# Kernel tuning notes

Hardware: AMD Instinct MI355X
Metric: run time of the kernel (lower is better)

Reference implementation:

```python
import jax, jax.numpy as jnp
import numpy as np

B, I, N = 1024, 128, 256
UNFOLDS = 6  # ode_solver_unfolds


def _sig(v, mu, sigma):
    # v: [B, D] -> [B, D, 1]; mu/sigma: [D, N] -> broadcast [B, D, N]
    return jax.nn.sigmoid(sigma * (v[..., None] - mu))


def setup_inputs() -> dict:
    key = jax.random.key(0)
    ks = jax.random.split(key, 12)
    u = lambda k, shape, lo, hi: jax.random.uniform(k, shape, jnp.float32, lo, hi)
    pm1 = lambda k, shape: (2.0 * jax.random.randint(k, shape, 0, 2) - 1.0).astype(jnp.float32)
    return {
        "inputs": jax.random.normal(ks[0], (B, I), jnp.float32),
        "state": jax.random.normal(ks[1], (B, N), jnp.float32) * 0.1,
        "input_w": jnp.ones((I,), jnp.float32),
        "input_b": jnp.zeros((I,), jnp.float32),
        "sensory_mu": u(ks[2], (I, N), 0.3, 0.8),
        "sensory_sigma": u(ks[3], (I, N), 3.0, 8.0),
        "sensory_W": u(ks[4], (I, N), 0.01, 1.0),
        "sensory_erev": pm1(ks[5], (I, N)),
        "mu": u(ks[6], (N, N), 0.3, 0.8),
        "sigma": u(ks[7], (N, N), 3.0, 8.0),
        "W": u(ks[8], (N, N), 0.01, 1.0),
        "erev": pm1(ks[9], (N, N)),
        "vleak": u(ks[10], (N,), -0.2, 0.2),
        "gleak": jnp.ones((N,), jnp.float32),   # gleak_init_min == gleak_init_max == 1.0
        "cm_t": jnp.full((N,), 0.5, jnp.float32),  # cm_init_min == cm_init_max == 0.5
    }


def reference(inputs, state, input_w, input_b, sensory_mu, sensory_sigma,
              sensory_W, sensory_erev, mu, sigma, W, erev, vleak, gleak, cm_t):
    # Affine input mapping
    x = inputs * input_w + input_b  # [B, I]
    # Sensory synapse activations (constant across unfolds)
    s_act = sensory_W * _sig(x, sensory_mu, sensory_sigma)  # [B, I, N]
    w_num_sensory = jnp.sum(s_act * sensory_erev, axis=1)   # [B, N]
    w_den_sensory = jnp.sum(s_act, axis=1)                  # [B, N]

    def step(v_pre, _):
        w_act = W * _sig(v_pre, mu, sigma)                  # [B, N, N]
        w_num = jnp.sum(w_act * erev, axis=1) + w_num_sensory
        w_den = jnp.sum(w_act, axis=1) + w_den_sensory
        numerator = cm_t * v_pre + gleak * vleak + w_num
        denominator = cm_t + gleak + w_den
        return numerator / denominator, None

    v_pre, _ = jax.lax.scan(step, state, None, length=UNFOLDS)
    # module returns (outputs, next_state) with outputs == next_state
    return v_pre
```

## Files before the change

### kernel.cpp

```cpp
#include <hip/hip_runtime.h>


#define LOG2E 1.44269504088896340f

constexpr int Bn = 1024;
constexpr int In = 128;
constexpr int Nn = 256;
constexpr int UNFOLDS = 6;

#if __has_builtin(__builtin_amdgcn_exp2f)
#define EXP2F(x) __builtin_amdgcn_exp2f(x)
#else
#define EXP2F(x) __exp2f(x)
#endif
#if __has_builtin(__builtin_amdgcn_rcpf)
#define RCPF(x) __builtin_amdgcn_rcpf(x)
#else
#define RCPF(x) (1.0f / (x))
#endif

__global__ __launch_bounds__(256) void pack_kernel(
    const float* __restrict__ mu, const float* __restrict__ sigma,
    const float* __restrict__ W, const float* __restrict__ erev,
    const float* __restrict__ smu, const float* __restrict__ ssigma,
    const float* __restrict__ sW, const float* __restrict__ serev,
    float4* __restrict__ Prec, float4* __restrict__ Psen) {
    int idx = blockIdx.x * 256 + threadIdx.x;
    if (idx < Nn * Nn) {
        float s = sigma[idx], m = mu[idx], w = W[idx], e = erev[idx];
        Prec[idx] = make_float4(s * LOG2E, s * m * LOG2E, w, w * e);
        return;
    }
    int j = idx - Nn * Nn;
    if (j < In * Nn) {
        float s = ssigma[j], m = smu[j], w = sW[j], e = serev[j];
        Psen[j] = make_float4(s * LOG2E, s * m * LOG2E, w, w * e);
    }
}

__global__ __launch_bounds__(256) void sensory_kernel(
    const float* __restrict__ inputs, const float* __restrict__ input_w,
    const float* __restrict__ input_b, const float4* __restrict__ Psen,
    float2* __restrict__ sens) {
    __shared__ float4 xs[In];
    __shared__ float2 part[4][4][64];

    const int tid = threadIdx.x;
    const int b0 = (blockIdx.x >> 2) * 4;
    const int n0 = (blockIdx.x & 3) * 64;

    for (int k = tid; k < 4 * In; k += 256) {
        int i = k >> 2, bb = k & 3;
        ((float*)xs)[i * 4 + bb] =
            inputs[(b0 + bb) * In + i] * input_w[i] + input_b[i];
    }
    __syncthreads();

    const int n_l = tid & 63;
    const int sl = tid >> 6;
    const float4* __restrict__ pp = Psen + n0 + n_l;

    float num[4] = {0.f, 0.f, 0.f, 0.f};
    float den[4] = {0.f, 0.f, 0.f, 0.f};
#pragma unroll 4
    for (int i = sl * 32; i < sl * 32 + 32; ++i) {
        float4 p = pp[i * Nn];
        float4 v = xs[i];
#pragma unroll
        for (int bb = 0; bb < 4; ++bb) {
            float vb = (bb == 0) ? v.x : (bb == 1) ? v.y : (bb == 2) ? v.z : v.w;
            float r = RCPF(1.0f + EXP2F(fmaf(-p.x, vb, p.y)));
            den[bb] += p.z * r;
            num[bb] += p.w * r;
        }
    }
#pragma unroll
    for (int bb = 0; bb < 4; ++bb)
        part[sl][bb][n_l] = make_float2(num[bb], den[bb]);
    __syncthreads();

    const int bb = tid >> 6, nl2 = tid & 63;
    float wn = 0.f, wd = 0.f;
#pragma unroll
    for (int s = 0; s < 4; ++s) {
        float2 v = part[s][bb][nl2];
        wn += v.x;
        wd += v.y;
    }
    sens[(b0 + bb) * Nn + n0 + nl2] = make_float2(wn, wd);
}

__global__ __launch_bounds__(256) void step_kernel(
    const float* __restrict__ vcur, const float4* __restrict__ Prec,
    const float2* __restrict__ sens, const float* __restrict__ vleak,
    const float* __restrict__ gleak, const float* __restrict__ cmt,
    float* __restrict__ vnext) {
    __shared__ float4 vt[Nn];
    __shared__ float2 part[4][4][64];

    const int tid = threadIdx.x;
    const int b0 = (blockIdx.x >> 2) * 4;
    const int n0 = (blockIdx.x & 3) * 64;

    for (int k = tid; k < 4 * Nn; k += 256) {
        int i = k >> 2, bb = k & 3;
        ((float*)vt)[i * 4 + bb] = vcur[(b0 + bb) * Nn + i];
    }
    __syncthreads();

    const int n_l = tid & 63;
    const int sl = tid >> 6;
    const float4* __restrict__ pp = Prec + n0 + n_l;

    float num[4] = {0.f, 0.f, 0.f, 0.f};
    float den[4] = {0.f, 0.f, 0.f, 0.f};
#pragma unroll 4
    for (int i = sl * 64; i < sl * 64 + 64; ++i) {
        float4 p = pp[i * Nn];
        float4 v = vt[i];
#pragma unroll
        for (int bb = 0; bb < 4; ++bb) {
            float vb = (bb == 0) ? v.x : (bb == 1) ? v.y : (bb == 2) ? v.z : v.w;
            float r = RCPF(1.0f + EXP2F(fmaf(-p.x, vb, p.y)));
            den[bb] += p.z * r;
            num[bb] += p.w * r;
        }
    }
#pragma unroll
    for (int bb = 0; bb < 4; ++bb)
        part[sl][bb][n_l] = make_float2(num[bb], den[bb]);
    __syncthreads();

    const int bb = tid >> 6, nl2 = tid & 63;
    const int n = n0 + nl2, b = b0 + bb;
    float wn = 0.f, wd = 0.f;
#pragma unroll
    for (int s = 0; s < 4; ++s) {
        float2 v = part[s][bb][nl2];
        wn += v.x;
        wd += v.y;
    }
    float2 sv = sens[b * Nn + n];
    float g = gleak[n], c = cmt[n], vl = vleak[n];
    float vp = vcur[b * Nn + n];
    vnext[b * Nn + n] = (c * vp + g * vl + wn + sv.x) / (c + g + wd + sv.y);
}

extern "C" void kernel_launch(void* const* d_in, const int* in_sizes, int n_in,
                              void* d_out, int out_size, void* d_ws, size_t ws_size,
                              hipStream_t stream) {
    const float* inputs   = (const float*)d_in[0];
    const float* state    = (const float*)d_in[1];
    const float* input_w  = (const float*)d_in[2];
    const float* input_b  = (const float*)d_in[3];
    const float* smu      = (const float*)d_in[4];
    const float* ssigma   = (const float*)d_in[5];
    const float* sW       = (const float*)d_in[6];
    const float* serev    = (const float*)d_in[7];
    const float* mu       = (const float*)d_in[8];
    const float* sigma    = (const float*)d_in[9];
    const float* W        = (const float*)d_in[10];
    const float* erev     = (const float*)d_in[11];
    const float* vleak    = (const float*)d_in[12];
    const float* gleak    = (const float*)d_in[13];
    const float* cmt      = (const float*)d_in[14];
    float* out = (float*)d_out;

    char* ws = (char*)d_ws;
    float4* Prec = (float4*)ws;
    float4* Psen = (float4*)(ws + (1u << 20));
    float2* sens = (float2*)(ws + (1u << 20) + (512u << 10));
    float*  vA   = (float*)(ws + (3u << 20) + (512u << 10));
    float*  vB   = (float*)(ws + (4u << 20) + (512u << 10));

    pack_kernel<<<(Nn * Nn + In * Nn + 255) / 256, 256, 0, stream>>>(
        mu, sigma, W, erev, smu, ssigma, sW, serev, Prec, Psen);

    sensory_kernel<<<1024, 256, 0, stream>>>(inputs, input_w, input_b, Psen, sens);

    const float* cur = state;
    for (int s = 0; s < UNFOLDS; ++s) {
        float* nxt = (s == UNFOLDS - 1) ? out : ((s & 1) ? vB : vA);
        step_kernel<<<1024, 256, 0, stream>>>(cur, Prec, sens, vleak, gleak, cmt, nxt);
        cur = nxt;
    }
}
```

Before: 202.1 us.

## Fuse sensory and all ODE unfold steps into a single persistent kernel

Replaces the separate sensory kernel and six per-step kernels with one kernel where each 1024-thread block owns four batch rows and iterates all unfolds, keeping the state in shared memory and the sensory sums in registers. This removes repeated kernel launches and the global round trips for the intermediate state and sensory terms. It also swaps the final division for a reciprocal approximation. In exchange it runs one large block per CU with fewer blocks overall, which can reduce latency hiding while streaming the recurrent parameters.

```diff
diff --git a/kernel.cpp b/kernel.cpp
--- a/kernel.cpp
+++ b/kernel.cpp
@@ -38,112 +38,99 @@
     }
 }
 
-__global__ __launch_bounds__(256) void sensory_kernel(
-    const float* __restrict__ inputs, const float* __restrict__ input_w,
-    const float* __restrict__ input_b, const float4* __restrict__ Psen,
-    float2* __restrict__ sens) {
+__global__ __launch_bounds__(1024, 1) void ltc_fused_kernel(
+    const float* __restrict__ inputs, const float* __restrict__ state,
+    const float* __restrict__ input_w, const float* __restrict__ input_b,
+    const float4* __restrict__ Psen, const float4* __restrict__ Prec,
+    const float* __restrict__ vleak, const float* __restrict__ gleak,
+    const float* __restrict__ cmt, float* __restrict__ out) {
+    __shared__ float4 vt[Nn];
+    __shared__ float2 part[4][4][Nn];
     __shared__ float4 xs[In];
-    __shared__ float2 part[4][4][64];
 
     const int tid = threadIdx.x;
-    const int b0 = (blockIdx.x >> 2) * 4;
-    const int n0 = (blockIdx.x & 3) * 64;
+    const int b0 = blockIdx.x * 4;
+    const int n = tid & 255;
+    const int ih = tid >> 8;
 
-    for (int k = tid; k < 4 * In; k += 256) {
-        int i = k >> 2, bb = k & 3;
+    float vp = state[(b0 + ih) * Nn + n];
+    ((float*)vt)[n * 4 + ih] = vp;
+    if (tid < 4 * In) {
+        int i = tid & 127, bb = tid >> 7;
         ((float*)xs)[i * 4 + bb] =
             inputs[(b0 + bb) * In + i] * input_w[i] + input_b[i];
     }
+    const float g = gleak[n], c = cmt[n];
+    const float gvl = g * vleak[n];
     __syncthreads();
 
-    const int n_l = tid & 63;
-    const int sl = tid >> 6;
-    const float4* __restrict__ pp = Psen + n0 + n_l;
+    float sens_n, sens_d;
+    {
+        float num[4] = {0.f, 0.f, 0.f, 0.f};
+        float den[4] = {0.f, 0.f, 0.f, 0.f};
+        const float4* __restrict__ pp = Psen + n;
+#pragma unroll 8
+        for (int i = ih * 32; i < ih * 32 + 32; ++i) {
+            float4 p = pp[i * Nn];
+            float4 v = xs[i];
+#pragma unroll
+            for (int bb = 0; bb < 4; ++bb) {
+                float vb = (bb == 0) ? v.x : (bb == 1) ? v.y : (bb == 2) ? v.z : v.w;
+                float r = RCPF(1.0f + EXP2F(fmaf(-p.x, vb, p.y)));
+                den[bb] += p.z * r;
+                num[bb] += p.w * r;
+            }
+        }
+#pragma unroll
+        for (int bb = 0; bb < 4; ++bb)
+            part[ih][bb][n] = make_float2(num[bb], den[bb]);
+        __syncthreads();
+        float wn = 0.f, wd = 0.f;
+#pragma unroll
+        for (int s = 0; s < 4; ++s) {
+            float2 v = part[s][ih][n];
+            wn += v.x;
+            wd += v.y;
+        }
+        sens_n = wn;
+        sens_d = wd;
+    }
 
-    float num[4] = {0.f, 0.f, 0.f, 0.f};
-    float den[4] = {0.f, 0.f, 0.f, 0.f};
-#pragma unroll 4
-    for (int i = sl * 32; i < sl * 32 + 32; ++i) {
-        float4 p = pp[i * Nn];
-        float4 v = xs[i];
+    const float4* __restrict__ pp = Prec + n;
+    for (int s = 0; s < UNFOLDS; ++s) {
+        __syncthreads();
+        float num[4] = {0.f, 0.f, 0.f, 0.f};
+        float den[4] = {0.f, 0.f, 0.f, 0.f};
+#pragma unroll 8
+        for (int i = ih * 64; i < ih * 64 + 64; ++i) {
+            float4 p = pp[i * Nn];
+            float4 v = vt[i];
 #pragma unroll
-        for (int bb = 0; bb < 4; ++bb) {
-            float vb = (bb == 0) ? v.x : (bb == 1) ? v.y : (bb == 2) ? v.z : v.w;
-            float r = RCPF(1.0f + EXP2F(fmaf(-p.x, vb, p.y)));
-            den[bb] += p.z * r;
-            num[bb] += p.w * r;
+            for (int bb = 0; bb < 4; ++bb) {
+                float vb = (bb == 0) ? v.x : (bb == 1) ? v.y : (bb == 2) ? v.z : v.w;
+                float r = RCPF(1.0f + EXP2F(fmaf(-p.x, vb, p.y)));
+                den[bb] += p.z * r;
+                num[bb] += p.w * r;
+            }
         }
+#pragma unroll
+        for (int bb = 0; bb < 4; ++bb)
+            part[ih][bb][n] = make_float2(num[bb], den[bb]);
+        __syncthreads();
+        float wn = sens_n, wd = sens_d;
+#pragma unroll
+        for (int s2 = 0; s2 < 4; ++s2) {
+            float2 v = part[s2][ih][n];
+            wn += v.x;
+            wd += v.y;
+        }
+        float res = (c * vp + gvl + wn) * RCPF(c + g + wd);
+        vp = res;
+        if (s == UNFOLDS - 1)
+            out[(b0 + ih) * Nn + n] = res;
+        else
+            ((float*)vt)[n * 4 + ih] = res;
     }
-#pragma unroll
-    for (int bb = 0; bb < 4; ++bb)
-        part[sl][bb][n_l] = make_float2(num[bb], den[bb]);
-    __syncthreads();
-
-    const int bb = tid >> 6, nl2 = tid & 63;
-    float wn = 0.f, wd = 0.f;
-#pragma unroll
-    for (int s = 0; s < 4; ++s) {
-        float2 v = part[s][bb][nl2];
-        wn += v.x;
-        wd += v.y;
-    }
-    sens[(b0 + bb) * Nn + n0 + nl2] = make_float2(wn, wd);
-}
-
-__global__ __launch_bounds__(256) void step_kernel(
-    const float* __restrict__ vcur, const float4* __restrict__ Prec,
-    const float2* __restrict__ sens, const float* __restrict__ vleak,
-    const float* __restrict__ gleak, const float* __restrict__ cmt,
-    float* __restrict__ vnext) {
-    __shared__ float4 vt[Nn];
-    __shared__ float2 part[4][4][64];
-
-    const int tid = threadIdx.x;
-    const int b0 = (blockIdx.x >> 2) * 4;
-    const int n0 = (blockIdx.x & 3) * 64;
-
-    for (int k = tid; k < 4 * Nn; k += 256) {
-        int i = k >> 2, bb = k & 3;
-        ((float*)vt)[i * 4 + bb] = vcur[(b0 + bb) * Nn + i];
-    }
-    __syncthreads();
-
-    const int n_l = tid & 63;
-    const int sl = tid >> 6;
-    const float4* __restrict__ pp = Prec + n0 + n_l;
-
-    float num[4] = {0.f, 0.f, 0.f, 0.f};
-    float den[4] = {0.f, 0.f, 0.f, 0.f};
-#pragma unroll 4
-    for (int i = sl * 64; i < sl * 64 + 64; ++i) {
-        float4 p = pp[i * Nn];
-        float4 v = vt[i];
-#pragma unroll
-        for (int bb = 0; bb < 4; ++bb) {
-            float vb = (bb == 0) ? v.x : (bb == 1) ? v.y : (bb == 2) ? v.z : v.w;
-            float r = RCPF(1.0f + EXP2F(fmaf(-p.x, vb, p.y)));
-            den[bb] += p.z * r;
-            num[bb] += p.w * r;
-        }
-    }
-#pragma unroll
-    for (int bb = 0; bb < 4; ++bb)
-        part[sl][bb][n_l] = make_float2(num[bb], den[bb]);
-    __syncthreads();
-
-    const int bb = tid >> 6, nl2 = tid & 63;
-    const int n = n0 + nl2, b = b0 + bb;
-    float wn = 0.f, wd = 0.f;
-#pragma unroll
-    for (int s = 0; s < 4; ++s) {
-        float2 v = part[s][bb][nl2];
-        wn += v.x;
-        wd += v.y;
-    }
-    float2 sv = sens[b * Nn + n];
-    float g = gleak[n], c = cmt[n], vl = vleak[n];
-    float vp = vcur[b * Nn + n];
-    vnext[b * Nn + n] = (c * vp + g * vl + wn + sv.x) / (c + g + wd + sv.y);
 }
 
 extern "C" void kernel_launch(void* const* d_in, const int* in_sizes, int n_in,
@@ -169,19 +156,10 @@
     char* ws = (char*)d_ws;
     float4* Prec = (float4*)ws;
     float4* Psen = (float4*)(ws + (1u << 20));
-    float2* sens = (float2*)(ws + (1u << 20) + (512u << 10));
-    float*  vA   = (float*)(ws + (3u << 20) + (512u << 10));
-    float*  vB   = (float*)(ws + (4u << 20) + (512u << 10));
 
     pack_kernel<<<(Nn * Nn + In * Nn + 255) / 256, 256, 0, stream>>>(
         mu, sigma, W, erev, smu, ssigma, sW, serev, Prec, Psen);
 
-    sensory_kernel<<<1024, 256, 0, stream>>>(inputs, input_w, input_b, Psen, sens);
-
-    const float* cur = state;
-    for (int s = 0; s < UNFOLDS; ++s) {
-        float* nxt = (s == UNFOLDS - 1) ? out : ((s & 1) ? vB : vA);
-        step_kernel<<<1024, 256, 0, stream>>>(cur, Prec, sens, vleak, gleak, cmt, nxt);
-        cur = nxt;
-    }
+    ltc_fused_kernel<<<Bn / 4, 1024, 0, stream>>>(
+        inputs, state, input_w, input_b, Psen, Prec, vleak, gleak, cmt, out);
 }
```

Measured after the change: 180.4 us. 1.12x faster.
